# Kernel optimization log

Hardware: AMD Instinct MI355X
Metric: run time of the kernel (lower is better)

## Reference

```python
import jax, jax.numpy as jnp
import numpy as np

B, N, DIM = 4, 4096, 512
H, DH = 8, 64
INNER = H * DH
M = 256            # num_landmarks (N % M == 0, so no padding branch)
PINV_ITERS = 6
KERNEL = 33
EPS = 1e-8


def moore_penrose_iter_pinv(x, iters=PINV_ITERS):
    # x: [b, h, m, m]
    abs_x = jnp.abs(x)
    col = abs_x.sum(axis=-1)
    row = abs_x.sum(axis=-2)
    z = jnp.swapaxes(x, -1, -2) / (jnp.max(col) * jnp.max(row) + 1e-8)
    I = jnp.eye(x.shape[-1], dtype=x.dtype)
    for _ in range(iters):
        xz = x @ z
        z = 0.25 * z @ (13 * I - xz @ (15 * I - xz @ (7 * I - xz)))
    return z


def setup_inputs() -> dict:
    key = jax.random.key(0)
    kx, kqkv, kout, kres = jax.random.split(key, 4)
    x = jax.random.normal(kx, (B, N, DIM), dtype=jnp.float32)
    w_qkv = jax.random.normal(kqkv, (DIM, 3 * INNER), dtype=jnp.float32) * (DIM ** -0.5)
    w_out = jax.random.normal(kout, (INNER, DIM), dtype=jnp.float32) * (INNER ** -0.5)
    # depthwise Conv2d(heads, heads, (33,1), groups=heads): weight [H, 1, 33, 1]
    w_res = jax.random.normal(kres, (H, 1, KERNEL, 1), dtype=jnp.float32) * (KERNEL ** -0.5)
    return {"x": x, "w_qkv": w_qkv, "w_out": w_out, "w_res": w_res}


def reference(x, w_qkv, w_out, w_res):
    b, n, _ = x.shape
    l = n // M  # tokens per landmark group
    scale = DH ** -0.5

    qkv = x @ w_qkv                                   # [b, n, 3*inner]
    q, k, v = jnp.split(qkv, 3, axis=-1)
    def to_heads(t):
        return t.reshape(b, n, H, DH).transpose(0, 2, 1, 3)  # [b, h, n, d]
    q, k, v = to_heads(q), to_heads(k), to_heads(v)
    q = q * scale

    # landmarks: mean over consecutive groups of l tokens
    q_land = q.reshape(b, H, M, l, DH).sum(axis=3) / l      # [b, h, m, d]
    k_land = k.reshape(b, H, M, l, DH).sum(axis=3) / l

    sim1 = jnp.einsum('bhid,bhjd->bhij', q, k_land)         # [b, h, n, m]
    sim2 = jnp.einsum('bhid,bhjd->bhij', q_land, k_land)    # [b, h, m, m]
    sim3 = jnp.einsum('bhid,bhjd->bhij', q_land, k)         # [b, h, m, n]

    attn1 = jax.nn.softmax(sim1, axis=-1)
    attn2 = jax.nn.softmax(sim2, axis=-1)
    attn3 = jax.nn.softmax(sim3, axis=-1)

    attn2_inv = moore_penrose_iter_pinv(attn2)
    out = attn1 @ (attn2_inv @ (attn3 @ v))                 # [b, h, n, d]

    # residual depthwise conv over sequence dim, per head channel
    res = jax.lax.conv_general_dilated(
        v, w_res, window_strides=(1, 1),
        padding=((KERNEL // 2, KERNEL // 2), (0, 0)),
        dimension_numbers=('NCHW', 'OIHW', 'NCHW'),
        feature_group_count=H)
    out = out + res

    out = out.transpose(0, 2, 1, 3).reshape(b, n, INNER)    # [b, n, inner]
    out = out @ w_out                                       # [b, n, dim]
    return out[:, -n:]
```

## Files before the change

### kernel.cpp

```cpp
#include <hip/hip_runtime.h>


typedef __attribute__((ext_vector_type(8))) short bf16x8;
typedef __attribute__((ext_vector_type(4))) float f32x4;

constexpr size_t O_XP  = 0;
constexpr size_t O_QP  = 8388608;
constexpr size_t O_KP  = 16777216;
constexpr size_t O_VT  = 25165824;
constexpr size_t O_QL  = 33554432;
constexpr size_t O_KL  = 34078720;
constexpr size_t O_QLP = 34603008;
constexpr size_t O_KLP = 35127296;
constexpr size_t O_A2  = 35651584;
constexpr size_t O_T1  = 37748736;
constexpr size_t O_RS3 = 38273024;
constexpr size_t O_SCAL= 38281216;
constexpr size_t O_CS  = 38281232;
constexpr size_t O_WQT = 38805520;
constexpr size_t O_WOT = 39591952;
constexpr size_t O_END = 39854096;

__device__ __forceinline__ void split2(float x, unsigned short& h,
                                       unsigned short& l) {
    unsigned u  = __float_as_uint(x);
    unsigned hb = (u + 0x7FFFu + ((u >> 16) & 1u)) & 0xFFFF0000u;
    h = (unsigned short)(hb >> 16);
    float d = x - __uint_as_float(hb);
    l = (unsigned short)(__float_as_uint(d) >> 16);
}

__device__ __forceinline__ float b2f(unsigned short s) {
    return __uint_as_float((unsigned)s << 16);
}

__device__ __forceinline__ f32x4 mfma3(bf16x8 ah, bf16x8 al, bf16x8 bh,
                                       bf16x8 bl, f32x4 c) {
    c = __builtin_amdgcn_mfma_f32_16x16x32_bf16(ah, bh, c, 0, 0, 0);
    c = __builtin_amdgcn_mfma_f32_16x16x32_bf16(ah, bl, c, 0, 0, 0);
    c = __builtin_amdgcn_mfma_f32_16x16x32_bf16(al, bh, c, 0, 0, 0);
    return c;
}

__device__ __forceinline__ void g2l16(const unsigned short* g,
                                      unsigned short* l) {
    __builtin_amdgcn_global_load_lds(
        (const __attribute__((address_space(1))) void*)g,
        (__attribute__((address_space(3))) void*)l, 16, 0, 0);
}

__device__ __forceinline__ void stage_split4(float4 av, unsigned short* H,
                                             unsigned short* L, int off) {
    unsigned short h0, h1, h2, h3, l0, l1, l2, l3;
    split2(av.x, h0, l0); split2(av.y, h1, l1);
    split2(av.z, h2, l2); split2(av.w, h3, l3);
    uint2 ph, pl;
    ph.x = (unsigned)h0 | ((unsigned)h1 << 16);
    ph.y = (unsigned)h2 | ((unsigned)h3 << 16);
    pl.x = (unsigned)l0 | ((unsigned)l1 << 16);
    pl.y = (unsigned)l2 | ((unsigned)l3 << 16);
    *(uint2*)&H[off] = ph;
    *(uint2*)&L[off] = pl;
}

__global__ void xsplit(const float* __restrict__ X,
                       unsigned short* __restrict__ Xh,
                       unsigned short* __restrict__ Xl) {
    int idx = blockIdx.x * 256 + threadIdx.x;
    float4 v = *(const float4*)(X + (size_t)idx * 4);
    stage_split4(v, Xh, Xl, idx * 4);
}

__global__ void wtrans2(const float* __restrict__ Wq,
                        const float* __restrict__ Wo,
                        unsigned short* __restrict__ QTh,
                        unsigned short* __restrict__ QTl,
                        unsigned short* __restrict__ OTh,
                        unsigned short* __restrict__ OTl) {
    int idx = blockIdx.x * 256 + threadIdx.x;
    unsigned short h, l;
    if (idx < 786432) {
        int n = idx >> 9, kk = idx & 511;
        split2(Wq[(size_t)kk * 1536 + n], h, l);
        QTh[idx] = h;
        QTl[idx] = l;
    } else {
        int j = idx - 786432;
        int n = j >> 9, kk = j & 511;
        split2(Wo[(size_t)kk * 512 + n], h, l);
        OTh[j] = h;
        OTl[j] = l;
    }
}

template <int EPI, int SC, bool WN, bool WTT>
__global__ __launch_bounds__(256) void mfma_gemm_p(
    const unsigned short* __restrict__ ANh, const unsigned short* __restrict__ ANl,
    const unsigned short* __restrict__ BTh, const unsigned short* __restrict__ BTl,
    unsigned short* __restrict__ CNh, unsigned short* __restrict__ CNl,
    unsigned short* __restrict__ CTh, unsigned short* __restrict__ CTl,
    float alpha, float beta, const float* __restrict__ scal) {
    __shared__ __align__(16) unsigned short Ah[64 * 32], Al[64 * 32];
    __shared__ __align__(16) unsigned short Bh[64 * 32], Bl[64 * 32];
    const int t = threadIdx.x;
    const int wave = t >> 6, lane = t & 63, lm = lane & 15, lq = lane >> 4;
    const int z = blockIdx.z;
    const int m0 = blockIdx.y * 64, n0 = blockIdx.x * 64;
    const size_t zo = (size_t)z * 65536;

    const unsigned short* gsrc;
    unsigned short* ldst;
    if (wave == 0)      { gsrc = ANh + zo + (size_t)m0 * 256; ldst = Ah; }
    else if (wave == 1) { gsrc = ANl + zo + (size_t)m0 * 256; ldst = Al; }
    else if (wave == 2) { gsrc = BTh + zo + (size_t)n0 * 256; ldst = Bh; }
    else                { gsrc = BTl + zo + (size_t)n0 * 256; ldst = Bl; }
    const int srow = lane >> 2, sko = (lane & 3) * 8;

    f32x4 acc[4];
#pragma unroll
    for (int j = 0; j < 4; ++j) acc[j] = (f32x4){0.f, 0.f, 0.f, 0.f};

    for (int kt = 0; kt < 256; kt += 32) {
#pragma unroll
        for (int c = 0; c < 4; ++c)
            g2l16(gsrc + (size_t)(c * 16 + srow) * 256 + kt + sko,
                  ldst + c * 512);
        __syncthreads();
        bf16x8 ah = *(const bf16x8*)&Ah[(wave * 16 + lm) * 32 + lq * 8];
        bf16x8 al = *(const bf16x8*)&Al[(wave * 16 + lm) * 32 + lq * 8];
#pragma unroll
        for (int j = 0; j < 4; ++j) {
            bf16x8 bh = *(const bf16x8*)&Bh[(j * 16 + lm) * 32 + lq * 8];
            bf16x8 bl = *(const bf16x8*)&Bl[(j * 16 + lm) * 32 + lq * 8];
            acc[j] = mfma3(ah, al, bh, bl, acc[j]);
        }
        __syncthreads();
    }

    const float scv = (SC != 0) ? 1.0f / (scal[0] + 1e-8f) : 1.0f;
    const float a = (SC == 1) ? scv : alpha;
    const int r0 = m0 + wave * 16 + lq * 4;
#pragma unroll
    for (int j = 0; j < 4; ++j) {
        int c = n0 + j * 16 + lm;
        float vals[4];
#pragma unroll
        for (int e = 0; e < 4; ++e) {
            float v = a * acc[j][e];
            if (EPI == 1) {
                size_t ao = zo + (size_t)(r0 + e) * 256 + c;
                v += beta * (b2f(ANh[ao]) + b2f(ANl[ao]));
            }
            if (SC == 2) v *= scv;
            vals[e] = v;
        }
        unsigned short hh[4], ll[4];
#pragma unroll
        for (int e = 0; e < 4; ++e) split2(vals[e], hh[e], ll[e]);
        if (WN) {
#pragma unroll
            for (int e = 0; e < 4; ++e) {
                size_t o = zo + (size_t)(r0 + e) * 256 + c;
                CNh[o] = hh[e];
                CNl[o] = ll[e];
            }
        }
        if (WTT) {
            uint2 ph, pl;
            ph.x = (unsigned)hh[0] | ((unsigned)hh[1] << 16);
            ph.y = (unsigned)hh[2] | ((unsigned)hh[3] << 16);
            pl.x = (unsigned)ll[0] | ((unsigned)ll[1] << 16);
            pl.y = (unsigned)ll[2] | ((unsigned)ll[3] << 16);
            *(uint2*)&CTh[zo + (size_t)c * 256 + r0] = ph;
            *(uint2*)&CTl[zo + (size_t)c * 256 + r0] = pl;
        }
    }
}

__device__ __forceinline__ void mt16(const float* As, const float* Bs,
                                     int ty4, int tx4, float (&acc)[4][4]) {
#pragma unroll
    for (int kk = 0; kk < 16; ++kk) {
        float4 a4 = *(const float4*)(As + kk * 68 + ty4);
        float4 b4 = *(const float4*)(Bs + kk * 68 + tx4);
        float aa[4] = {a4.x, a4.y, a4.z, a4.w};
        float bb[4] = {b4.x, b4.y, b4.z, b4.w};
#pragma unroll
        for (int u = 0; u < 4; ++u)
#pragma unroll
            for (int w = 0; w < 4; ++w)
                acc[u][w] += aa[u] * bb[w];
    }
}

__global__ __launch_bounds__(256) void t2_gemm(
    const unsigned short* __restrict__ ANh, const unsigned short* __restrict__ ANl,
    const float* __restrict__ t1, const float* __restrict__ rs3,
    unsigned short* __restrict__ t2Th, unsigned short* __restrict__ t2Tl) {
    __shared__ float As[16 * 68];
    __shared__ float Bs[16 * 68];
    const int t  = threadIdx.x;
    const int z  = blockIdx.z;
    const int m0 = blockIdx.y * 64;
    const size_t zo = (size_t)z * 65536;
    const float* Bb = t1 + (size_t)z * 16384;
    const int tx4 = (t & 15) * 4;
    const int ty4 = (t >> 4) * 4;
    const int ar  = t >> 2, ak = (t & 3) * 4;
    const int bkr = t >> 4, bc4 = (t & 15) * 4;
    float acc[4][4] = {};
    for (int kt = 0; kt < 256; kt += 16) {
        uint2 h2 = *(const uint2*)(ANh + zo + (size_t)(m0 + ar) * 256 + kt + ak);
        uint2 l2 = *(const uint2*)(ANl + zo + (size_t)(m0 + ar) * 256 + kt + ak);
        const unsigned short* hp = (const unsigned short*)&h2;
        const unsigned short* lp = (const unsigned short*)&l2;
        float4 av = make_float4(b2f(hp[0]) + b2f(lp[0]), b2f(hp[1]) + b2f(lp[1]),
                                b2f(hp[2]) + b2f(lp[2]), b2f(hp[3]) + b2f(lp[3]));
        float4 bv = *(const float4*)(Bb + (size_t)(kt + bkr) * 64 + bc4);
        float rr = 1.0f / rs3[z * 256 + kt + bkr];
        bv.x *= rr; bv.y *= rr; bv.z *= rr; bv.w *= rr;
        As[(ak + 0) * 68 + ar] = av.x;
        As[(ak + 1) * 68 + ar] = av.y;
        As[(ak + 2) * 68 + ar] = av.z;
        As[(ak + 3) * 68 + ar] = av.w;
        *(float4*)(Bs + bkr * 68 + bc4) = bv;
        __syncthreads();
        mt16(As, Bs, ty4, tx4, acc);
        __syncthreads();
    }
#pragma unroll
    for (int w = 0; w < 4; ++w) {
        unsigned short hh[4], ll[4];
#pragma unroll
        for (int u = 0; u < 4; ++u) split2(acc[u][w], hh[u], ll[u]);
        uint2 ph, pl;
        ph.x = (unsigned)hh[0] | ((unsigned)hh[1] << 16);
        ph.y = (unsigned)hh[2] | ((unsigned)hh[3] << 16);
        pl.x = (unsigned)ll[0] | ((unsigned)ll[1] << 16);
        pl.y = (unsigned)ll[2] | ((unsigned)ll[3] << 16);
        size_t off = (size_t)z * 16384 + (size_t)(tx4 + w) * 256 + m0 + ty4;
        *(uint2*)&t2Th[off] = ph;
        *(uint2*)&t2Tl[off] = pl;
    }
}

__global__ __launch_bounds__(256) void mfma_qkv(
    const unsigned short* __restrict__ Xh_, const unsigned short* __restrict__ Xl_,
    const unsigned short* __restrict__ WTh, const unsigned short* __restrict__ WTl,
    unsigned short* __restrict__ qh, unsigned short* __restrict__ ql,
    unsigned short* __restrict__ kh, unsigned short* __restrict__ kl,
    unsigned short* __restrict__ vTh, unsigned short* __restrict__ vTl) {
    __shared__ __align__(16) unsigned short Ah[128 * 32], Al[128 * 32];
    __shared__ __align__(16) unsigned short Bh[128 * 32], Bl[128 * 32];
    const int t = threadIdx.x;
    const int wave = t >> 6, lane = t & 63, lm = lane & 15, lq = lane >> 4;
    int orig = blockIdx.y * 12 + blockIdx.x;
    int wg = (orig & 7) * 192 + (orig >> 3);
    const int m0 = (wg / 12) * 128, n0 = (wg % 12) * 128;
    const int mb = (wave >> 1) * 64, nb = (wave & 1) * 64;

    const unsigned short* gsrc;
    unsigned short* ldst;
    if (wave == 0)      { gsrc = Xh_ + (size_t)m0 * 512; ldst = Ah; }
    else if (wave == 1) { gsrc = Xl_ + (size_t)m0 * 512; ldst = Al; }
    else if (wave == 2) { gsrc = WTh + (size_t)n0 * 512; ldst = Bh; }
    else                { gsrc = WTl + (size_t)n0 * 512; ldst = Bl; }
    const int srow = lane >> 2, sko = (lane & 3) * 8;

    f32x4 acc[4][4];
#pragma unroll
    for (int i = 0; i < 4; ++i)
#pragma unroll
        for (int j = 0; j < 4; ++j) acc[i][j] = (f32x4){0.f, 0.f, 0.f, 0.f};

    for (int kt = 0; kt < 512; kt += 32) {
#pragma unroll
        for (int c = 0; c < 8; ++c)
            g2l16(gsrc + (size_t)(c * 16 + srow) * 512 + kt + sko,
                  ldst + c * 512);
        __syncthreads();
        bf16x8 ah[4], al[4], bh[4], bl[4];
#pragma unroll
        for (int i = 0; i < 4; ++i) {
            ah[i] = *(const bf16x8*)&Ah[(mb + i * 16 + lm) * 32 + lq * 8];
            al[i] = *(const bf16x8*)&Al[(mb + i * 16 + lm) * 32 + lq * 8];
        }
#pragma unroll
        for (int j = 0; j < 4; ++j) {
            bh[j] = *(const bf16x8*)&Bh[(nb + j * 16 + lm) * 32 + lq * 8];
            bl[j] = *(const bf16x8*)&Bl[(nb + j * 16 + lm) * 32 + lq * 8];
        }
#pragma unroll
        for (int i = 0; i < 4; ++i)
#pragma unroll
            for (int j = 0; j < 4; ++j)
                acc[i][j] = mfma3(ah[i], al[i], bh[j], bl[j], acc[i][j]);
        __syncthreads();
    }
#pragma unroll
    for (int i = 0; i < 4; ++i)
#pragma unroll
        for (int j = 0; j < 4; ++j) {
            int r0 = m0 + mb + i * 16 + lq * 4;
            int c  = n0 + nb + j * 16 + lm;
            int which = c >> 9, h = (c >> 6) & 7, d = c & 63;
            int b = r0 >> 12, nbase = r0 & 4095;
            if (which == 2) {
                unsigned short hh[4], ll[4];
#pragma unroll
                for (int e = 0; e < 4; ++e) split2(acc[i][j][e], hh[e], ll[e]);
                uint2 ph, pl;
                ph.x = (unsigned)hh[0] | ((unsigned)hh[1] << 16);
                ph.y = (unsigned)hh[2] | ((unsigned)hh[3] << 16);
                pl.x = (unsigned)ll[0] | ((unsigned)ll[1] << 16);
                pl.y = (unsigned)ll[2] | ((unsigned)ll[3] << 16);
                size_t off = ((size_t)(b * 8 + h) * 64 + d) * 4096 + nbase;
                *(uint2*)&vTh[off] = ph;
                *(uint2*)&vTl[off] = pl;
            } else {
                unsigned short* Ph = which ? kh : qh;
                unsigned short* Pl = which ? kl : ql;
                float sc = which ? 1.0f : 0.125f;
#pragma unroll
                for (int e = 0; e < 4; ++e) {
                    unsigned short hh, ll;
                    split2(acc[i][j][e] * sc, hh, ll);
                    size_t off = (size_t)(b * 8 + h) * 262144 +
                                 (size_t)(nbase + e) * 64 + d;
                    Ph[off] = hh;
                    Pl[off] = ll;
                }
            }
        }
}

__global__ __launch_bounds__(256) void mfma_final(
    const unsigned short* __restrict__ OHh, const unsigned short* __restrict__ OHl,
    const unsigned short* __restrict__ WTh, const unsigned short* __restrict__ WTl,
    float* __restrict__ out) {
    __shared__ __align__(16) unsigned short Ah[128 * 32], Al[128 * 32];
    __shared__ __align__(16) unsigned short Bh[128 * 32], Bl[128 * 32];
    const int t = threadIdx.x;
    const int wave = t >> 6, lane = t & 63, lm = lane & 15, lq = lane >> 4;
    int orig = blockIdx.y * 4 + blockIdx.x;
    int wg = (orig & 7) * 64 + (orig >> 3);
    const int m0 = (wg >> 2) * 128, n0 = (wg & 3) * 128;
    const int mb = (wave >> 1) * 64, nb = (wave & 1) * 64;

    const bool isA = wave < 2;
    const unsigned short* gA = (wave == 0) ? OHh : OHl;
    const unsigned short* gB = (wave == 2) ? WTh : WTl;
    unsigned short* ldst = (wave == 0) ? Ah : (wave == 1) ? Al
                         : (wave == 2) ? Bh : Bl;
    const int srow = lane >> 2, sko = (lane & 3) * 8;
    int gb[8], gn[8];
#pragma unroll
    for (int c = 0; c < 8; ++c) {
        int gr = m0 + c * 16 + srow;
        gb[c] = gr >> 12;
        gn[c] = gr & 4095;
    }

    f32x4 acc[4][4];
#pragma unroll
    for (int i = 0; i < 4; ++i)
#pragma unroll
        for (int j = 0; j < 4; ++j) acc[i][j] = (f32x4){0.f, 0.f, 0.f, 0.f};

    for (int kt = 0; kt < 512; kt += 32) {
        if (isA) {
            int kk = kt + sko;
            size_t koff = (size_t)(kk >> 6) * 262144 + (kk & 63);
#pragma unroll
            for (int c = 0; c < 8; ++c)
                g2l16(gA + (size_t)gb[c] * 2097152 + koff +
                          (size_t)gn[c] * 64,
                      ldst + c * 512);
        } else {
#pragma unroll
            for (int c = 0; c < 8; ++c)
                g2l16(gB + (size_t)(n0 + c * 16 + srow) * 512 + kt + sko,
                      ldst + c * 512);
        }
        __syncthreads();
        bf16x8 ah[4], al[4], bh[4], bl[4];
#pragma unroll
        for (int i = 0; i < 4; ++i) {
            ah[i] = *(const bf16x8*)&Ah[(mb + i * 16 + lm) * 32 + lq * 8];
            al[i] = *(const bf16x8*)&Al[(mb + i * 16 + lm) * 32 + lq * 8];
        }
#pragma unroll
        for (int j = 0; j < 4; ++j) {
            bh[j] = *(const bf16x8*)&Bh[(nb + j * 16 + lm) * 32 + lq * 8];
            bl[j] = *(const bf16x8*)&Bl[(nb + j * 16 + lm) * 32 + lq * 8];
        }
#pragma unroll
        for (int i = 0; i < 4; ++i)
#pragma unroll
            for (int j = 0; j < 4; ++j)
                acc[i][j] = mfma3(ah[i], al[i], bh[j], bl[j], acc[i][j]);
        __syncthreads();
    }
#pragma unroll
    for (int i = 0; i < 4; ++i)
#pragma unroll
        for (int j = 0; j < 4; ++j) {
            int r0 = m0 + mb + i * 16 + lq * 4;
            int c  = n0 + nb + j * 16 + lm;
#pragma unroll
            for (int e = 0; e < 4; ++e)
                out[(size_t)(r0 + e) * 512 + c] = acc[i][j][e];
        }
}

__global__ __launch_bounds__(256) void attn3v_mfma(
    const unsigned short* __restrict__ qlh, const unsigned short* __restrict__ qll,
    const unsigned short* __restrict__ kh_, const unsigned short* __restrict__ kl_,
    const unsigned short* __restrict__ vTh, const unsigned short* __restrict__ vTl,
    float* __restrict__ t1, float* __restrict__ rs3) {
    __shared__ unsigned short Qh[4608], Ql[4608];
    __shared__ unsigned short Kh[4608], Kl[4608];
    __shared__ unsigned short Eh[4608], El[4608];
    const int t = threadIdx.x;
    const int wave = t >> 6, lane = t & 63, lm = lane & 15, lq = lane >> 4;
    const int bz = blockIdx.z, m0 = blockIdx.y * 64, c0 = blockIdx.x * 8;
    const unsigned short* qhb = qlh + (size_t)bz * 16384;
    const unsigned short* qlb = qll + (size_t)bz * 16384;
    const unsigned short* khb = kh_ + (size_t)bz * 262144;
    const unsigned short* klb = kl_ + (size_t)bz * 262144;
    const unsigned short* vhb = vTh + (size_t)bz * 262144;
    const unsigned short* vlb = vTl + (size_t)bz * 262144;
#pragma unroll
    for (int r = 0; r < 2; ++r) {
        int id = t + r * 256, row = id >> 3, ko = (id & 7) * 8;
        *(uint4*)&Qh[row * 72 + ko] =
            *(const uint4*)(qhb + (size_t)(m0 + row) * 64 + ko);
        *(uint4*)&Ql[row * 72 + ko] =
            *(const uint4*)(qlb + (size_t)(m0 + row) * 64 + ko);
    }
    f32x4 acc[4];
#pragma unroll
    for (int j = 0; j < 4; ++j) acc[j] = (f32x4){0.f, 0.f, 0.f, 0.f};
    float rsum[4] = {0.f, 0.f, 0.f, 0.f};
    __syncthreads();

    for (int c = c0; c < c0 + 8; ++c) {
        const int tok0 = c * 64;
#pragma unroll
        for (int r = 0; r < 2; ++r) {
            int id = t + r * 256, row = id >> 3, ko = (id & 7) * 8;
            *(uint4*)&Kh[row * 72 + ko] =
                *(const uint4*)(khb + (size_t)(tok0 + row) * 64 + ko);
            *(uint4*)&Kl[row * 72 + ko] =
                *(const uint4*)(klb + (size_t)(tok0 + row) * 64 + ko);
        }
        __syncthreads();
        bf16x8 a0  = *(const bf16x8*)&Qh[(wave * 16 + lm) * 72 + lq * 8];
        bf16x8 a0l = *(const bf16x8*)&Ql[(wave * 16 + lm) * 72 + lq * 8];
        bf16x8 a1  = *(const bf16x8*)&Qh[(wave * 16 + lm) * 72 + 32 + lq * 8];
        bf16x8 a1l = *(const bf16x8*)&Ql[(wave * 16 + lm) * 72 + 32 + lq * 8];
        f32x4 s[4];
#pragma unroll
        for (int j = 0; j < 4; ++j) s[j] = (f32x4){0.f, 0.f, 0.f, 0.f};
#pragma unroll
        for (int j = 0; j < 4; ++j) {
            bf16x8 b0  = *(const bf16x8*)&Kh[(j * 16 + lm) * 72 + lq * 8];
            bf16x8 b0l = *(const bf16x8*)&Kl[(j * 16 + lm) * 72 + lq * 8];
            bf16x8 b1  = *(const bf16x8*)&Kh[(j * 16 + lm) * 72 + 32 + lq * 8];
            bf16x8 b1l = *(const bf16x8*)&Kl[(j * 16 + lm) * 72 + 32 + lq * 8];
            s[j] = mfma3(a0, a0l, b0, b0l, s[j]);
            s[j] = mfma3(a1, a1l, b1, b1l, s[j]);
        }
        __syncthreads();
#pragma unroll
        for (int j = 0; j < 4; ++j)
#pragma unroll
            for (int e = 0; e < 4; ++e) {
                float ev = __expf(s[j][e]);
                rsum[e] += ev;
                unsigned short h, l;
                split2(ev, h, l);
                int off = (wave * 16 + lq * 4 + e) * 72 + j * 16 + lm;
                Eh[off] = h;
                El[off] = l;
            }
#pragma unroll
        for (int r = 0; r < 2; ++r) {
            int id = t + r * 256, dh = id >> 3, t8 = (id & 7) * 8;
            *(uint4*)&Kh[dh * 72 + t8] =
                *(const uint4*)(vhb + (size_t)dh * 4096 + tok0 + t8);
            *(uint4*)&Kl[dh * 72 + t8] =
                *(const uint4*)(vlb + (size_t)dh * 4096 + tok0 + t8);
        }
        __syncthreads();
        bf16x8 e0  = *(const bf16x8*)&Eh[(wave * 16 + lm) * 72 + lq * 8];
        bf16x8 e0l = *(const bf16x8*)&El[(wave * 16 + lm) * 72 + lq * 8];
        bf16x8 e1  = *(const bf16x8*)&Eh[(wave * 16 + lm) * 72 + 32 + lq * 8];
        bf16x8 e1l = *(const bf16x8*)&El[(wave * 16 + lm) * 72 + 32 + lq * 8];
#pragma unroll
        for (int j = 0; j < 4; ++j) {
            bf16x8 v0  = *(const bf16x8*)&Kh[(j * 16 + lm) * 72 + lq * 8];
            bf16x8 v0l = *(const bf16x8*)&Kl[(j * 16 + lm) * 72 + lq * 8];
            bf16x8 v1  = *(const bf16x8*)&Kh[(j * 16 + lm) * 72 + 32 + lq * 8];
            bf16x8 v1l = *(const bf16x8*)&Kl[(j * 16 + lm) * 72 + 32 + lq * 8];
            acc[j] = mfma3(e0, e0l, v0, v0l, acc[j]);
            acc[j] = mfma3(e1, e1l, v1, v1l, acc[j]);
        }
        __syncthreads();
    }
    float* t1b = t1 + (size_t)bz * 16384;
#pragma unroll
    for (int j = 0; j < 4; ++j)
#pragma unroll
        for (int e = 0; e < 4; ++e)
            atomicAdd(t1b + (size_t)(m0 + wave * 16 + lq * 4 + e) * 64 +
                          j * 16 + lm,
                      acc[j][e]);
#pragma unroll
    for (int e = 0; e < 4; ++e) {
        float vs = rsum[e];
        for (int mm = 1; mm < 16; mm <<= 1) vs += __shfl_xor(vs, mm);
        if (lm == 0)
            atomicAdd(rs3 + bz * 256 + m0 + wave * 16 + lq * 4 + e, vs);
    }
}

__global__ __launch_bounds__(256) void attn1t2_conv(
    const unsigned short* __restrict__ qh_, const unsigned short* __restrict__ ql_,
    const unsigned short* __restrict__ klh, const unsigned short* __restrict__ kll,
    const unsigned short* __restrict__ t2Th, const unsigned short* __restrict__ t2Tl,
    const unsigned short* __restrict__ vTh, const unsigned short* __restrict__ vTl,
    const float* __restrict__ wres,
    unsigned short* __restrict__ OHh, unsigned short* __restrict__ OHl) {
    __shared__ __align__(16) unsigned short SH[27648];
    unsigned short* Qh = SH;
    unsigned short* Ql = SH + 4608;
    unsigned short* Kh = SH + 9216;
    unsigned short* Kl = SH + 13824;
    unsigned short* Eh = SH + 18432;
    unsigned short* El = SH + 23040;
    __shared__ float Ws[33];
    const int t = threadIdx.x;
    const int wave = t >> 6, lane = t & 63, lm = lane & 15, lq = lane >> 4;
    const int bz = blockIdx.y, m0 = blockIdx.x * 64;
    if (t < 33) Ws[t] = wres[(bz & 7) * 33 + t];
    const unsigned short* qhb = qh_ + (size_t)bz * 262144;
    const unsigned short* qlb = ql_ + (size_t)bz * 262144;
    const unsigned short* khb = klh + (size_t)bz * 16384;
    const unsigned short* klb = kll + (size_t)bz * 16384;
    const unsigned short* t2h = t2Th + (size_t)bz * 16384;
    const unsigned short* t2l = t2Tl + (size_t)bz * 16384;
#pragma unroll
    for (int r = 0; r < 2; ++r) {
        int id = t + r * 256, row = id >> 3, ko = (id & 7) * 8;
        *(uint4*)&Qh[row * 72 + ko] =
            *(const uint4*)(qhb + (size_t)(m0 + row) * 64 + ko);
        *(uint4*)&Ql[row * 72 + ko] =
            *(const uint4*)(qlb + (size_t)(m0 + row) * 64 + ko);
    }
    f32x4 acc[4];
#pragma unroll
    for (int j = 0; j < 4; ++j) acc[j] = (f32x4){0.f, 0.f, 0.f, 0.f};
    float rsum[4] = {0.f, 0.f, 0.f, 0.f};
    __syncthreads();

    for (int lc = 0; lc < 4; ++lc) {
        const int l0 = lc * 64;
#pragma unroll
        for (int r = 0; r < 2; ++r) {
            int id = t + r * 256, row = id >> 3, ko = (id & 7) * 8;
            *(uint4*)&Kh[row * 72 + ko] =
                *(const uint4*)(khb + (size_t)(l0 + row) * 64 + ko);
            *(uint4*)&Kl[row * 72 + ko] =
                *(const uint4*)(klb + (size_t)(l0 + row) * 64 + ko);
        }
        __syncthreads();
        bf16x8 a0  = *(const bf16x8*)&Qh[(wave * 16 + lm) * 72 + lq * 8];
        bf16x8 a0l = *(const bf16x8*)&Ql[(wave * 16 + lm) * 72 + lq * 8];
        bf16x8 a1  = *(const bf16x8*)&Qh[(wave * 16 + lm) * 72 + 32 + lq * 8];
        bf16x8 a1l = *(const bf16x8*)&Ql[(wave * 16 + lm) * 72 + 32 + lq * 8];
        f32x4 s[4];
#pragma unroll
        for (int j = 0; j < 4; ++j) s[j] = (f32x4){0.f, 0.f, 0.f, 0.f};
#pragma unroll
        for (int j = 0; j < 4; ++j) {
            bf16x8 b0  = *(const bf16x8*)&Kh[(j * 16 + lm) * 72 + lq * 8];
            bf16x8 b0l = *(const bf16x8*)&Kl[(j * 16 + lm) * 72 + lq * 8];
            bf16x8 b1  = *(const bf16x8*)&Kh[(j * 16 + lm) * 72 + 32 + lq * 8];
            bf16x8 b1l = *(const bf16x8*)&Kl[(j * 16 + lm) * 72 + 32 + lq * 8];
            s[j] = mfma3(a0, a0l, b0, b0l, s[j]);
            s[j] = mfma3(a1, a1l, b1, b1l, s[j]);
        }
        __syncthreads();
#pragma unroll
        for (int j = 0; j < 4; ++j)
#pragma unroll
            for (int e = 0; e < 4; ++e) {
                float ev = __expf(s[j][e]);
                rsum[e] += ev;
                unsigned short h, l;
                split2(ev, h, l);
                int off = (wave * 16 + lq * 4 + e) * 72 + j * 16 + lm;
                Eh[off] = h;
                El[off] = l;
            }
#pragma unroll
        for (int r = 0; r < 2; ++r) {
            int id = t + r * 256, dh = id >> 3, t8 = (id & 7) * 8;
            *(uint4*)&Kh[dh * 72 + t8] =
                *(const uint4*)(t2h + (size_t)dh * 256 + l0 + t8);
            *(uint4*)&Kl[dh * 72 + t8] =
                *(const uint4*)(t2l + (size_t)dh * 256 + l0 + t8);
        }
        __syncthreads();
        bf16x8 e0  = *(const bf16x8*)&Eh[(wave * 16 + lm) * 72 + lq * 8];
        bf16x8 e0l = *(const bf16x8*)&El[(wave * 16 + lm) * 72 + lq * 8];
        bf16x8 e1  = *(const bf16x8*)&Eh[(wave * 16 + lm) * 72 + 32 + lq * 8];
        bf16x8 e1l = *(const bf16x8*)&El[(wave * 16 + lm) * 72 + 32 + lq * 8];
#pragma unroll
        for (int j = 0; j < 4; ++j) {
            bf16x8 v0  = *(const bf16x8*)&Kh[(j * 16 + lm) * 72 + lq * 8];
            bf16x8 v0l = *(const bf16x8*)&Kl[(j * 16 + lm) * 72 + lq * 8];
            bf16x8 v1  = *(const bf16x8*)&Kh[(j * 16 + lm) * 72 + 32 + lq * 8];
            bf16x8 v1l = *(const bf16x8*)&Kl[(j * 16 + lm) * 72 + 32 + lq * 8];
            acc[j] = mfma3(e0, e0l, v0, v0l, acc[j]);
            acc[j] = mfma3(e1, e1l, v1, v1l, acc[j]);
        }
        __syncthreads();
    }
    float rinv[4];
#pragma unroll
    for (int e = 0; e < 4; ++e) {
        float vs = rsum[e];
        for (int mm = 1; mm < 16; mm <<= 1) vs += __shfl_xor(vs, mm);
        rinv[e] = 1.0f / vs;
    }

    __syncthreads();
    float* Vs = (float*)SH;
    const unsigned short* vhb = vTh + (size_t)bz * 262144;
    const unsigned short* vlb = vTl + (size_t)bz * 262144;
#pragma unroll
    for (int r = 0; r < 3; ++r) {
        int id = t + r * 256;
        int d = id / 12, ch = id - d * 12;
        int n = m0 - 16 + ch * 8;
        uint4 h4 = make_uint4(0u, 0u, 0u, 0u);
        uint4 l4 = make_uint4(0u, 0u, 0u, 0u);
        if ((unsigned)n < 4096u) {
            h4 = *(const uint4*)(vhb + (size_t)d * 4096 + n);
            l4 = *(const uint4*)(vlb + (size_t)d * 4096 + n);
        }
        const unsigned short* hp = (const unsigned short*)&h4;
        const unsigned short* lp = (const unsigned short*)&l4;
#pragma unroll
        for (int i = 0; i < 8; ++i)
            Vs[(ch * 8 + i) * 65 + d] = b2f(hp[i]) + b2f(lp[i]);
    }
    __syncthreads();
    unsigned short* Hh = OHh + (size_t)bz * 262144;
    unsigned short* Hl = OHl + (size_t)bz * 262144;
    const int rbase = wave * 16 + lq * 4;
#pragma unroll
    for (int j = 0; j < 4; ++j) {
        int cc = j * 16 + lm;
        float w[36];
#pragma unroll
        for (int u = 0; u < 36; ++u) w[u] = Vs[(rbase + u) * 65 + cc];
#pragma unroll
        for (int e = 0; e < 4; ++e) {
            float cv = 0.f;
#pragma unroll
            for (int tt = 0; tt < 33; ++tt) cv += w[e + tt] * Ws[tt];
            float o = acc[j][e] * rinv[e] + cv;
            unsigned short hh, ll;
            split2(o, hh, ll);
            size_t off = (size_t)(m0 + rbase + e) * 64 + cc;
            Hh[off] = hh;
            Hl[off] = ll;
        }
    }
}

__global__ __launch_bounds__(256) void gemm_a2(
    const float* __restrict__ A, const float* __restrict__ B,
    float* __restrict__ C) {
    __shared__ float As[16 * 68];
    __shared__ float Bs[16 * 68];
    const int t  = threadIdx.x;
    const int z  = blockIdx.z;
    const int m0 = blockIdx.y * 64;
    const int n0 = blockIdx.x * 64;
    const float* Ab = A + (size_t)z * 16384;
    const float* Bb = B + (size_t)z * 16384;
    float*       Cb = C + (size_t)z * 65536;
    const int tx4 = (t & 15) * 4;
    const int ty4 = (t >> 4) * 4;
    const int ar  = t >> 2, ak = (t & 3) * 4;
    float acc[4][4] = {};
    for (int kt = 0; kt < 64; kt += 16) {
        float4 av = *(const float4*)(Ab + (size_t)(m0 + ar) * 64 + kt + ak);
        float4 bv = *(const float4*)(Bb + (size_t)(n0 + ar) * 64 + kt + ak);
        As[(ak + 0) * 68 + ar] = av.x;
        As[(ak + 1) * 68 + ar] = av.y;
        As[(ak + 2) * 68 + ar] = av.z;
        As[(ak + 3) * 68 + ar] = av.w;
        Bs[(ak + 0) * 68 + ar] = bv.x;
        Bs[(ak + 1) * 68 + ar] = bv.y;
        Bs[(ak + 2) * 68 + ar] = bv.z;
        Bs[(ak + 3) * 68 + ar] = bv.w;
        __syncthreads();
        mt16(As, Bs, ty4, tx4, acc);
        __syncthreads();
    }
#pragma unroll
    for (int u = 0; u < 4; ++u) {
        int row = m0 + ty4 + u;
        *(float4*)(Cb + (size_t)row * 256 + n0 + tx4) =
            make_float4(acc[u][0], acc[u][1], acc[u][2], acc[u][3]);
    }
}

__global__ void zero_f(float* __restrict__ p, int n) {
    int i = blockIdx.x * 256 + threadIdx.x;
    if (i < n) p[i] = 0.f;
}

__global__ void landmark_mean2(
    const unsigned short* __restrict__ qh, const unsigned short* __restrict__ ql,
    const unsigned short* __restrict__ kh, const unsigned short* __restrict__ kl,
    float* __restrict__ qland, float* __restrict__ kland,
    unsigned short* __restrict__ qlh, unsigned short* __restrict__ qll,
    unsigned short* __restrict__ klh, unsigned short* __restrict__ kll) {
    int o = blockIdx.x * 256 + threadIdx.x;
    bool isq = o < 524288;
    int oo = isq ? o : o - 524288;
    const unsigned short* sh = isq ? qh : kh;
    const unsigned short* sl = isq ? ql : kl;
    float* dst = isq ? qland : kland;
    unsigned short* dh = isq ? qlh : klh;
    unsigned short* dl = isq ? qll : kll;
    int d = oo & 63, m = (oo >> 6) & 255, bh = oo >> 14;
    size_t base = (size_t)bh * 262144 + (size_t)m * 1024 + d;
    float acc = 0.f;
#pragma unroll
    for (int j = 0; j < 16; ++j)
        acc += b2f(sh[base + j * 64]) + b2f(sl[base + j * 64]);
    float v = acc * (1.0f / 16.0f);
    dst[oo] = v;
    unsigned short h, l;
    split2(v, h, l);
    dh[oo] = h;
    dl[oo] = l;
}

__global__ void softmax_fused(const float* __restrict__ a,
                              unsigned short* __restrict__ A2Ph,
                              unsigned short* __restrict__ A2Pl,
                              unsigned short* __restrict__ A2Th,
                              unsigned short* __restrict__ A2Tl,
                              float* __restrict__ colsum) {
    __shared__ float red[256];
    int row = blockIdx.x, t = threadIdx.x;
    float v = a[(size_t)row * 256 + t];
    red[t] = v;
    __syncthreads();
    for (int s = 128; s > 0; s >>= 1) {
        if (t < s) red[t] = fmaxf(red[t], red[t + s]);
        __syncthreads();
    }
    float mx = red[0];
    __syncthreads();
    float e = __expf(v - mx);
    red[t] = e;
    __syncthreads();
    for (int s = 128; s > 0; s >>= 1) {
        if (t < s) red[t] += red[t + s];
        __syncthreads();
    }
    float val = e / red[0];
    int z = row >> 8, r = row & 255;
    atomicAdd(&colsum[z * 256 + t], val);
    unsigned short h, l;
    split2(val, h, l);
    size_t zo = (size_t)z * 65536;
    A2Ph[zo + (size_t)r * 256 + t] = h;
    A2Pl[zo + (size_t)r * 256 + t] = l;
    A2Th[zo + (size_t)t * 256 + r] = h;
    A2Tl[zo + (size_t)t * 256 + r] = l;
}

__global__ void scal_max(const float* __restrict__ colsum,
                         float* __restrict__ scal) {
    __shared__ float red[256];
    int t = threadIdx.x;
    red[t] = colsum[blockIdx.x * 256 + t];
    __syncthreads();
    for (int s = 128; s > 0; s >>= 1) {
        if (t < s) red[t] = fmaxf(red[t], red[t + s]);
        __syncthreads();
    }
    if (t == 0) atomicMax((unsigned int*)&scal[0], __float_as_uint(red[0]));
}

extern "C" void kernel_launch(void* const* d_in, const int* in_sizes, int n_in,
                              void* d_out, int out_size, void* d_ws, size_t ws_size,
                              hipStream_t stream) {
    const float* x     = (const float*)d_in[0];
    const float* w_qkv = (const float*)d_in[1];
    const float* w_out = (const float*)d_in[2];
    const float* w_res = (const float*)d_in[3];
    float* out = (float*)d_out;
    float* ws  = (float*)d_ws;

    unsigned short* Xh  = (unsigned short*)(ws + O_XP);
    unsigned short* Xl  = Xh + 8388608;
    unsigned short* qh  = (unsigned short*)(ws + O_QP);
    unsigned short* ql  = qh + 8388608;
    unsigned short* kh  = (unsigned short*)(ws + O_KP);
    unsigned short* kl  = kh + 8388608;
    unsigned short* vTh = (unsigned short*)(ws + O_VT);
    unsigned short* vTl = vTh + 8388608;
    unsigned short* qlh = (unsigned short*)(ws + O_QLP);
    unsigned short* qll = qlh + 524288;
    unsigned short* klh = (unsigned short*)(ws + O_KLP);
    unsigned short* kll = klh + 524288;

    float* qland = ws + O_QL;
    float* kland = ws + O_KL;
    float* attn2 = ws + O_A2;
    float* t1    = ws + O_T1;
    float* rs3   = ws + O_RS3;
    float* scal  = ws + O_SCAL;
    float* colsum= ws + O_CS;

    unsigned short* PBu  = (unsigned short*)(ws + O_KP);
    unsigned short* A2Ph = PBu + 0;
    unsigned short* A2Pl = PBu + 2097152;
    unsigned short* XZNh = PBu + 4194304;
    unsigned short* XZNl = PBu + 6291456;
    unsigned short* XZTh = PBu + 8388608;
    unsigned short* XZTl = PBu + 10485760;
    unsigned short* Y1Th = PBu + 12582912;
    unsigned short* Y1Tl = PBu + 14680064;
    unsigned short* XRu  = (unsigned short*)(ws + O_XP);
    unsigned short* ZNah = XRu + 0;
    unsigned short* ZNal = XRu + 2097152;
    unsigned short* ZNbh = XRu + 4194304;
    unsigned short* ZNbl = XRu + 6291456;
    unsigned short* ZTh_ = XRu + 8388608;
    unsigned short* ZTl_ = XRu + 10485760;
    unsigned short* Y2Th = XRu + 12582912;
    unsigned short* Y2Tl = XRu + 14680064;
    unsigned short* A2Th = ZNah;
    unsigned short* A2Tl = ZNal;
    unsigned short* t2Th = (unsigned short*)(ws + O_QL);
    unsigned short* t2Tl = t2Th + 524288;
    unsigned short* OHh = PBu;
    unsigned short* OHl = PBu + 8388608;

    unsigned short* WQTh = (unsigned short*)(ws + O_WQT);
    unsigned short* WQTl = WQTh + 786432;
    unsigned short* WOTh = (unsigned short*)(ws + O_WOT);
    unsigned short* WOTl = WOTh + 262144;

    zero_f<<<2113, 256, 0, stream>>>(t1, 540688);
    wtrans2<<<4096, 256, 0, stream>>>(w_qkv, w_out, WQTh, WQTl, WOTh, WOTl);
    xsplit<<<8192, 256, 0, stream>>>(x, Xh, Xl);

    mfma_qkv<<<dim3(12, 128), 256, 0, stream>>>(Xh, Xl, WQTh, WQTl,
                                                qh, ql, kh, kl, vTh, vTl);

    landmark_mean2<<<4096, 256, 0, stream>>>(qh, ql, kh, kl, qland, kland,
                                             qlh, qll, klh, kll);

    attn3v_mfma<<<dim3(8, 4, 32), 256, 0, stream>>>(qlh, qll, kh, kl,
                                                    vTh, vTl, t1, rs3);

    gemm_a2<<<dim3(4, 4, 32), 256, 0, stream>>>(qland, kland, attn2);
    softmax_fused<<<8192, 256, 0, stream>>>(attn2, A2Ph, A2Pl, A2Th, A2Tl,
                                            colsum);
    scal_max<<<32, 256, 0, stream>>>(colsum, scal);

    unsigned short* ZNh[2] = {ZNah, ZNbh};
    unsigned short* ZNl[2] = {ZNal, ZNbl};
    int cur = 0;
    const dim3 pg(4, 4, 32);
    for (int it = 0; it < 6; ++it) {
        if (it == 0) {
            mfma_gemm_p<0, 1, true, true><<<pg, 256, 0, stream>>>(
                A2Ph, A2Pl, A2Ph, A2Pl, XZNh, XZNl, XZTh, XZTl,
                0.f, 0.f, scal);
        } else {
            mfma_gemm_p<0, 0, true, true><<<pg, 256, 0, stream>>>(
                A2Ph, A2Pl, ZTh_, ZTl_, XZNh, XZNl, XZTh, XZTl,
                1.f, 0.f, scal);
        }
        mfma_gemm_p<1, 0, false, true><<<pg, 256, 0, stream>>>(
            XZNh, XZNl, XZTh, XZTl, nullptr, nullptr, Y1Th, Y1Tl,
            -1.f, 7.f, scal);
        mfma_gemm_p<1, 0, false, true><<<pg, 256, 0, stream>>>(
            XZNh, XZNl, Y1Th, Y1Tl, nullptr, nullptr, Y2Th, Y2Tl,
            -1.f, 15.f, scal);
        if (it == 0) {
            mfma_gemm_p<1, 2, true, true><<<pg, 256, 0, stream>>>(
                A2Th, A2Tl, Y2Th, Y2Tl, ZNbh, ZNbl, ZTh_, ZTl_,
                -0.25f, 3.25f, scal);
            cur = 1;
        } else {
            mfma_gemm_p<1, 0, true, true><<<pg, 256, 0, stream>>>(
                ZNh[cur], ZNl[cur], Y2Th, Y2Tl, ZNh[1 - cur], ZNl[1 - cur],
                ZTh_, ZTl_, -0.25f, 3.25f, scal);
            cur = 1 - cur;
        }
    }

    t2_gemm<<<dim3(1, 4, 32), 256, 0, stream>>>(ZNh[0], ZNl[0], t1, rs3,
                                                t2Th, t2Tl);

    attn1t2_conv<<<dim3(64, 32), 256, 0, stream>>>(qh, ql, klh, kll,
                                                   t2Th, t2Tl, vTh, vTl,
                                                   w_res, OHh, OHl);

    mfma_final<<<dim3(4, 128), 256, 0, stream>>>(OHh, OHl, WOTh, WOTl, out);

    (void)in_sizes; (void)n_in; (void)out_size; (void)ws_size;
}
```

Before: 777.5 us.

## Double-buffer LDS tiles in the MFMA GEMM kernels to overlap loads with compute

Splits the shared-memory A/B tiles of the pinv GEMM, QKV projection and output projection kernels into two buffers. Each iteration issues the global-to-LDS copy for the next K slice before running MFMAs on the current one, and drops one barrier per iteration. This is meant to hide global load latency behind matrix math. It doubles LDS use per block, which may lower occupancy, and its correctness depends on how g2l16 completes relative to the remaining barrier.

```diff
diff --git a/kernel.cpp b/kernel.cpp
--- a/kernel.cpp
+++ b/kernel.cpp
@@ -100,8 +100,8 @@
     unsigned short* __restrict__ CNh, unsigned short* __restrict__ CNl,
     unsigned short* __restrict__ CTh, unsigned short* __restrict__ CTl,
     float alpha, float beta, const float* __restrict__ scal) {
-    __shared__ __align__(16) unsigned short Ah[64 * 32], Al[64 * 32];
-    __shared__ __align__(16) unsigned short Bh[64 * 32], Bl[64 * 32];
+    __shared__ __align__(16) unsigned short Ah[2][2048], Al[2][2048];
+    __shared__ __align__(16) unsigned short Bh[2][2048], Bl[2][2048];
     const int t = threadIdx.x;
     const int wave = t >> 6, lane = t & 63, lm = lane & 15, lq = lane >> 4;
     const int z = blockIdx.z;
@@ -109,32 +109,39 @@
     const size_t zo = (size_t)z * 65536;
 
     const unsigned short* gsrc;
-    unsigned short* ldst;
+    unsigned short (*ldst)[2048];
     if (wave == 0)      { gsrc = ANh + zo + (size_t)m0 * 256; ldst = Ah; }
     else if (wave == 1) { gsrc = ANl + zo + (size_t)m0 * 256; ldst = Al; }
     else if (wave == 2) { gsrc = BTh + zo + (size_t)n0 * 256; ldst = Bh; }
     else                { gsrc = BTl + zo + (size_t)n0 * 256; ldst = Bl; }
     const int srow = lane >> 2, sko = (lane & 3) * 8;
 
-    f32x4 acc[4];
-#pragma unroll
-    for (int j = 0; j < 4; ++j) acc[j] = (f32x4){0.f, 0.f, 0.f, 0.f};
-
-    for (int kt = 0; kt < 256; kt += 32) {
+    auto stage = [&](int b, int kt) {
 #pragma unroll
         for (int c = 0; c < 4; ++c)
             g2l16(gsrc + (size_t)(c * 16 + srow) * 256 + kt + sko,
-                  ldst + c * 512);
-        __syncthreads();
-        bf16x8 ah = *(const bf16x8*)&Ah[(wave * 16 + lm) * 32 + lq * 8];
-        bf16x8 al = *(const bf16x8*)&Al[(wave * 16 + lm) * 32 + lq * 8];
+                  &ldst[b][c * 512]);
+    };
+
+    f32x4 acc[4];
+#pragma unroll
+    for (int j = 0; j < 4; ++j) acc[j] = (f32x4){0.f, 0.f, 0.f, 0.f};
+
+    stage(0, 0);
+    __syncthreads();
+    int cur = 0;
+    for (int kt = 0; kt < 256; kt += 32) {
+        if (kt + 32 < 256) stage(cur ^ 1, kt + 32);
+        bf16x8 ah = *(const bf16x8*)&Ah[cur][(wave * 16 + lm) * 32 + lq * 8];
+        bf16x8 al = *(const bf16x8*)&Al[cur][(wave * 16 + lm) * 32 + lq * 8];
 #pragma unroll
         for (int j = 0; j < 4; ++j) {
-            bf16x8 bh = *(const bf16x8*)&Bh[(j * 16 + lm) * 32 + lq * 8];
-            bf16x8 bl = *(const bf16x8*)&Bl[(j * 16 + lm) * 32 + lq * 8];
+            bf16x8 bh = *(const bf16x8*)&Bh[cur][(j * 16 + lm) * 32 + lq * 8];
+            bf16x8 bl = *(const bf16x8*)&Bl[cur][(j * 16 + lm) * 32 + lq * 8];
             acc[j] = mfma3(ah, al, bh, bl, acc[j]);
         }
         __syncthreads();
+        cur ^= 1;
     }
 
     const float scv = (SC != 0) ? 1.0f / (scal[0] + 1e-8f) : 1.0f;
@@ -250,8 +257,8 @@
     unsigned short* __restrict__ qh, unsigned short* __restrict__ ql,
     unsigned short* __restrict__ kh, unsigned short* __restrict__ kl,
     unsigned short* __restrict__ vTh, unsigned short* __restrict__ vTl) {
-    __shared__ __align__(16) unsigned short Ah[128 * 32], Al[128 * 32];
-    __shared__ __align__(16) unsigned short Bh[128 * 32], Bl[128 * 32];
+    __shared__ __align__(16) unsigned short Ah[2][4096], Al[2][4096];
+    __shared__ __align__(16) unsigned short Bh[2][4096], Bl[2][4096];
     const int t = threadIdx.x;
     const int wave = t >> 6, lane = t & 63, lm = lane & 15, lq = lane >> 4;
     int orig = blockIdx.y * 12 + blockIdx.x;
@@ -260,35 +267,41 @@
     const int mb = (wave >> 1) * 64, nb = (wave & 1) * 64;
 
     const unsigned short* gsrc;
-    unsigned short* ldst;
+    unsigned short (*ldst)[4096];
     if (wave == 0)      { gsrc = Xh_ + (size_t)m0 * 512; ldst = Ah; }
     else if (wave == 1) { gsrc = Xl_ + (size_t)m0 * 512; ldst = Al; }
     else if (wave == 2) { gsrc = WTh + (size_t)n0 * 512; ldst = Bh; }
     else                { gsrc = WTl + (size_t)n0 * 512; ldst = Bl; }
     const int srow = lane >> 2, sko = (lane & 3) * 8;
 
-    f32x4 acc[4][4];
-#pragma unroll
-    for (int i = 0; i < 4; ++i)
-#pragma unroll
-        for (int j = 0; j < 4; ++j) acc[i][j] = (f32x4){0.f, 0.f, 0.f, 0.f};
-
-    for (int kt = 0; kt < 512; kt += 32) {
+    auto stage = [&](int b, int kt) {
 #pragma unroll
         for (int c = 0; c < 8; ++c)
             g2l16(gsrc + (size_t)(c * 16 + srow) * 512 + kt + sko,
-                  ldst + c * 512);
-        __syncthreads();
+                  &ldst[b][c * 512]);
+    };
+
+    f32x4 acc[4][4];
+#pragma unroll
+    for (int i = 0; i < 4; ++i)
+#pragma unroll
+        for (int j = 0; j < 4; ++j) acc[i][j] = (f32x4){0.f, 0.f, 0.f, 0.f};
+
+    stage(0, 0);
+    __syncthreads();
+    int cur = 0;
+    for (int kt = 0; kt < 512; kt += 32) {
+        if (kt + 32 < 512) stage(cur ^ 1, kt + 32);
         bf16x8 ah[4], al[4], bh[4], bl[4];
 #pragma unroll
         for (int i = 0; i < 4; ++i) {
-            ah[i] = *(const bf16x8*)&Ah[(mb + i * 16 + lm) * 32 + lq * 8];
-            al[i] = *(const bf16x8*)&Al[(mb + i * 16 + lm) * 32 + lq * 8];
+            ah[i] = *(const bf16x8*)&Ah[cur][(mb + i * 16 + lm) * 32 + lq * 8];
+            al[i] = *(const bf16x8*)&Al[cur][(mb + i * 16 + lm) * 32 + lq * 8];
         }
 #pragma unroll
         for (int j = 0; j < 4; ++j) {
-            bh[j] = *(const bf16x8*)&Bh[(nb + j * 16 + lm) * 32 + lq * 8];
-            bl[j] = *(const bf16x8*)&Bl[(nb + j * 16 + lm) * 32 + lq * 8];
+            bh[j] = *(const bf16x8*)&Bh[cur][(nb + j * 16 + lm) * 32 + lq * 8];
+            bl[j] = *(const bf16x8*)&Bl[cur][(nb + j * 16 + lm) * 32 + lq * 8];
         }
 #pragma unroll
         for (int i = 0; i < 4; ++i)
@@ -296,6 +309,7 @@
             for (int j = 0; j < 4; ++j)
                 acc[i][j] = mfma3(ah[i], al[i], bh[j], bl[j], acc[i][j]);
         __syncthreads();
+        cur ^= 1;
     }
 #pragma unroll
     for (int i = 0; i < 4; ++i)
@@ -338,8 +352,8 @@
     const unsigned short* __restrict__ OHh, const unsigned short* __restrict__ OHl,
     const unsigned short* __restrict__ WTh, const unsigned short* __restrict__ WTl,
     float* __restrict__ out) {
-    __shared__ __align__(16) unsigned short Ah[128 * 32], Al[128 * 32];
-    __shared__ __align__(16) unsigned short Bh[128 * 32], Bl[128 * 32];
+    __shared__ __align__(16) unsigned short Ah[2][4096], Al[2][4096];
+    __shared__ __align__(16) unsigned short Bh[2][4096], Bl[2][4096];
     const int t = threadIdx.x;
     const int wave = t >> 6, lane = t & 63, lm = lane & 15, lq = lane >> 4;
     int orig = blockIdx.y * 4 + blockIdx.x;
@@ -350,8 +364,8 @@
     const bool isA = wave < 2;
     const unsigned short* gA = (wave == 0) ? OHh : OHl;
     const unsigned short* gB = (wave == 2) ? WTh : WTl;
-    unsigned short* ldst = (wave == 0) ? Ah : (wave == 1) ? Al
-                         : (wave == 2) ? Bh : Bl;
+    unsigned short (*ldst)[4096] = (wave == 0) ? Ah : (wave == 1) ? Al
+                                 : (wave == 2) ? Bh : Bl;
     const int srow = lane >> 2, sko = (lane & 3) * 8;
     int gb[8], gn[8];
 #pragma unroll
@@ -361,13 +375,7 @@
         gn[c] = gr & 4095;
     }
 
-    f32x4 acc[4][4];
-#pragma unroll
-    for (int i = 0; i < 4; ++i)
-#pragma unroll
-        for (int j = 0; j < 4; ++j) acc[i][j] = (f32x4){0.f, 0.f, 0.f, 0.f};
-
-    for (int kt = 0; kt < 512; kt += 32) {
+    auto stage = [&](int b, int kt) {
         if (isA) {
             int kk = kt + sko;
             size_t koff = (size_t)(kk >> 6) * 262144 + (kk & 63);
@@ -375,24 +383,36 @@
             for (int c = 0; c < 8; ++c)
                 g2l16(gA + (size_t)gb[c] * 2097152 + koff +
                           (size_t)gn[c] * 64,
-                      ldst + c * 512);
+                      &ldst[b][c * 512]);
         } else {
 #pragma unroll
             for (int c = 0; c < 8; ++c)
                 g2l16(gB + (size_t)(n0 + c * 16 + srow) * 512 + kt + sko,
-                      ldst + c * 512);
-        }
-        __syncthreads();
+                      &ldst[b][c * 512]);
+        }
+    };
+
+    f32x4 acc[4][4];
+#pragma unroll
+    for (int i = 0; i < 4; ++i)
+#pragma unroll
+        for (int j = 0; j < 4; ++j) acc[i][j] = (f32x4){0.f, 0.f, 0.f, 0.f};
+
+    stage(0, 0);
+    __syncthreads();
+    int cur = 0;
+    for (int kt = 0; kt < 512; kt += 32) {
+        if (kt + 32 < 512) stage(cur ^ 1, kt + 32);
         bf16x8 ah[4], al[4], bh[4], bl[4];
 #pragma unroll
         for (int i = 0; i < 4; ++i) {
-            ah[i] = *(const bf16x8*)&Ah[(mb + i * 16 + lm) * 32 + lq * 8];
-            al[i] = *(const bf16x8*)&Al[(mb + i * 16 + lm) * 32 + lq * 8];
+            ah[i] = *(const bf16x8*)&Ah[cur][(mb + i * 16 + lm) * 32 + lq * 8];
+            al[i] = *(const bf16x8*)&Al[cur][(mb + i * 16 + lm) * 32 + lq * 8];
         }
 #pragma unroll
         for (int j = 0; j < 4; ++j) {
-            bh[j] = *(const bf16x8*)&Bh[(nb + j * 16 + lm) * 32 + lq * 8];
-            bl[j] = *(const bf16x8*)&Bl[(nb + j * 16 + lm) * 32 + lq * 8];
+            bh[j] = *(const bf16x8*)&Bh[cur][(nb + j * 16 + lm) * 32 + lq * 8];
+            bl[j] = *(const bf16x8*)&Bl[cur][(nb + j * 16 + lm) * 32 + lq * 8];
         }
 #pragma unroll
         for (int i = 0; i < 4; ++i)
@@ -400,6 +420,7 @@
             for (int j = 0; j < 4; ++j)
                 acc[i][j] = mfma3(ah[i], al[i], bh[j], bl[j], acc[i][j]);
         __syncthreads();
+        cur ^= 1;
     }
 #pragma unroll
     for (int i = 0; i < 4; ++i)
```

Result: no change. 765.3 us (-1.6%).
